# Kernel optimization log

Measured on AMD Instinct MI355X. Metric: run time of the kernel, lower is better.

The kernel has to match this reference:

```python
import jax, jax.numpy as jnp
import numpy as np
from jax import lax

N_GAUSS = 4096


def setup_inputs() -> dict:
    key = jax.random.key(0)
    k1, k2, k3, k4 = jax.random.split(key, 4)
    return {
        "_xyz": jax.random.normal(k1, (N_GAUSS, 3), dtype=jnp.float32),
        "_scaling": jax.random.normal(k2, (N_GAUSS, 3), dtype=jnp.float32),
        "_rotation": jax.random.normal(k3, (N_GAUSS, 4), dtype=jnp.float32),
        "_opacity": jax.random.normal(k4, (N_GAUSS, 1), dtype=jnp.float32),
        "resolution": 64,
        "num_blocks": 16,
    }


def _extract_fields(_xyz, _scaling, _rotation, _opacity, resolution, num_blocks):
    relax_ratio = 1.5
    block_size = 2.0 / num_blocks
    split_size = resolution // num_blocks

    # opacity activation + threshold mask (kept dense; masked gaussians get 0 weight)
    opacities = jax.nn.sigmoid(_opacity)[:, 0]  # [N]
    keep = opacities > 0.005
    opa = jnp.where(keep, opacities, 0.0)

    BIG = jnp.float32(1e10)
    mn = jnp.min(jnp.where(keep[:, None], _xyz, BIG), axis=0)
    mx = jnp.max(jnp.where(keep[:, None], _xyz, -BIG), axis=0)
    center = (mn + mx) / 2
    scale = 1.8 / jnp.max(mx - mn)
    xyzs = (_xyz - center) * scale           # [N,3] normalized positions
    stds = jnp.exp(_scaling) * scale         # [N,3] scaling activation * scale

    # covariance from scaling+rotation: L = R @ diag(s); C = L L^T
    q = _rotation / jnp.linalg.norm(_rotation, axis=1, keepdims=True)
    r, x, y, z = q[:, 0], q[:, 1], q[:, 2], q[:, 3]
    R = jnp.stack([
        jnp.stack([1 - 2 * (y * y + z * z), 2 * (x * y - r * z), 2 * (x * z + r * y)], -1),
        jnp.stack([2 * (x * y + r * z), 1 - 2 * (x * x + z * z), 2 * (y * z - r * x)], -1),
        jnp.stack([2 * (x * z - r * y), 2 * (y * z + r * x), 1 - 2 * (x * x + y * y)], -1),
    ], axis=1)                               # [N,3,3]
    L = R * stds[:, None, :]                 # R @ diag(s)
    C = jnp.einsum('nij,nkj->nik', L, L)     # [N,3,3]
    a, b, c = C[:, 0, 0], C[:, 0, 1], C[:, 0, 2]
    d, e, f = C[:, 1, 1], C[:, 1, 2], C[:, 2, 2]

    # analytic 3x3 symmetric inverse (precomputed per gaussian)
    inv_det = 1.0 / (a * d * f + 2 * e * c * b - e * e * a - c * c * d - b * b * f + 1e-24)
    inv_a = (d * f - e * e) * inv_det
    inv_b = (e * c - b * f) * inv_det
    inv_c = (e * b - c * d) * inv_det
    inv_d = (a * f - c * c) * inv_det
    inv_e = (b * c - e * a) * inv_det
    inv_f = (a * d - b * b) * inv_det

    lin = jnp.linspace(-1.0, 1.0, resolution).astype(jnp.float32)
    nb = num_blocks
    bi, bj, bk = jnp.meshgrid(jnp.arange(nb), jnp.arange(nb), jnp.arange(nb), indexing='ij')
    blocks = jnp.stack([bi.ravel(), bj.ravel(), bk.ravel()], axis=1)  # [nb^3, 3]
    off = jnp.arange(split_size)
    relax = block_size * relax_ratio

    def block_val(blk):
        xs = lin[blk[0] * split_size + off]
        ys = lin[blk[1] * split_size + off]
        zs = lin[blk[2] * split_size + off]
        xx, yy, zz = jnp.meshgrid(xs, ys, zs, indexing='ij')
        pts = jnp.stack([xx.ravel(), yy.ravel(), zz.ravel()], axis=-1)  # [S^3, 3]
        vmin = pts.min(0) - relax
        vmax = pts.max(0) + relax
        inside = jnp.all((xyzs < vmax) & (xyzs > vmin), axis=1)  # [N]
        w_opa = jnp.where(inside, opa, 0.0)                      # [N]
        dxyz = pts[:, None, :] - xyzs[None, :, :]                # [S^3, N, 3]
        px, py, pz = dxyz[..., 0], dxyz[..., 1], dxyz[..., 2]
        power = (-0.5 * (px * px * inv_a + py * py * inv_d + pz * pz * inv_f)
                 - px * py * inv_b - px * pz * inv_c - py * pz * inv_e)
        power = jnp.where(power > 0, jnp.float32(-1e10), power)
        val = jnp.sum(w_opa * jnp.exp(power), axis=1)            # [S^3]
        return val.reshape(split_size, split_size, split_size)

    vals = lax.map(block_val, blocks)  # [nb^3, S, S, S]
    occ = (vals.reshape(nb, nb, nb, split_size, split_size, split_size)
               .transpose(0, 3, 1, 4, 2, 5)
               .reshape(resolution, resolution, resolution))
    return occ


def reference(_xyz, _scaling, _rotation, _opacity, resolution, num_blocks):
    return _extract_fields(_xyz, _scaling, _rotation, _opacity, resolution, num_blocks)
```

## Files before the change

kernel.cpp:

```cpp
#include <hip/hip_runtime.h>

#define NG 4096
#define RELAX 0.1875f
#define KEEPTH -5.2933049f

__device__ __forceinline__ float linf(int i) { return -1.0f + (2.0f/63.0f)*(float)i; }
__device__ __forceinline__ int cperm(int i) { return (i & 1) ? 7 + ((i+1)>>1) : 7 - (i>>1); }

template<int T>
__device__ __forceinline__ float4 block_minmax_cs(
    const float4* __restrict__ xyz4, const float4* __restrict__ op4,
    int tid, float (*s_r)[6])
{
  float mn0=1e10f, mn1=1e10f, mn2=1e10f;
  float mx0=-1e10f, mx1=-1e10f, mx2=-1e10f;
  #pragma unroll
  for (int t = 0; t < NG/4/T; ++t) {
    const int G = t*T + tid;
    float4 v0 = xyz4[3*G+0], v1 = xyz4[3*G+1], v2 = xyz4[3*G+2];
    float4 oo = op4[G];
    if (oo.x > KEEPTH) { mn0=fminf(mn0,v0.x); mx0=fmaxf(mx0,v0.x);
                         mn1=fminf(mn1,v0.y); mx1=fmaxf(mx1,v0.y);
                         mn2=fminf(mn2,v0.z); mx2=fmaxf(mx2,v0.z); }
    if (oo.y > KEEPTH) { mn0=fminf(mn0,v0.w); mx0=fmaxf(mx0,v0.w);
                         mn1=fminf(mn1,v1.x); mx1=fmaxf(mx1,v1.x);
                         mn2=fminf(mn2,v1.y); mx2=fmaxf(mx2,v1.y); }
    if (oo.z > KEEPTH) { mn0=fminf(mn0,v1.z); mx0=fmaxf(mx0,v1.z);
                         mn1=fminf(mn1,v1.w); mx1=fmaxf(mx1,v1.w);
                         mn2=fminf(mn2,v2.x); mx2=fmaxf(mx2,v2.x); }
    if (oo.w > KEEPTH) { mn0=fminf(mn0,v2.y); mx0=fmaxf(mx0,v2.y);
                         mn1=fminf(mn1,v2.z); mx1=fmaxf(mx1,v2.z);
                         mn2=fminf(mn2,v2.w); mx2=fmaxf(mx2,v2.w); }
  }
  #pragma unroll
  for (int s = 1; s < 64; s <<= 1) {
    mn0 = fminf(mn0, __shfl_xor(mn0, s)); mx0 = fmaxf(mx0, __shfl_xor(mx0, s));
    mn1 = fminf(mn1, __shfl_xor(mn1, s)); mx1 = fmaxf(mx1, __shfl_xor(mx1, s));
    mn2 = fminf(mn2, __shfl_xor(mn2, s)); mx2 = fmaxf(mx2, __shfl_xor(mx2, s));
  }
  if ((tid & 63) == 0) {
    const int w = tid >> 6;
    s_r[w][0]=mn0; s_r[w][1]=mn1; s_r[w][2]=mn2;
    s_r[w][3]=mx0; s_r[w][4]=mx1; s_r[w][5]=mx2;
  }
  __syncthreads();
  mn0 = s_r[0][0]; mn1 = s_r[0][1]; mn2 = s_r[0][2];
  mx0 = s_r[0][3]; mx1 = s_r[0][4]; mx2 = s_r[0][5];
  #pragma unroll
  for (int w = 1; w < T/64; ++w) {
    mn0 = fminf(mn0, s_r[w][0]); mn1 = fminf(mn1, s_r[w][1]); mn2 = fminf(mn2, s_r[w][2]);
    mx0 = fmaxf(mx0, s_r[w][3]); mx1 = fmaxf(mx1, s_r[w][4]); mx2 = fmaxf(mx2, s_r[w][5]);
  }
  return make_float4((mn0+mx0)*0.5f, (mn1+mx1)*0.5f, (mn2+mx2)*0.5f,
                     1.8f/fmaxf(mx0-mn0, fmaxf(mx1-mn1, mx2-mn2)));
}

__device__ __forceinline__ void transform_one(
    const float* __restrict__ xyz, const float* __restrict__ scal,
    const float* __restrict__ rot, const float* __restrict__ opac,
    int g, float cx, float cy, float cz, float sc,
    float4* __restrict__ pos, float4* __restrict__ inv)
{
  float o = opac[g];
  float sig = 1.0f/(1.0f + __expf(-o));
  float opa = (sig > 0.005f) ? sig : 0.0f;
  float xs = (xyz[3*g+0]-cx)*sc;
  float ys = (xyz[3*g+1]-cy)*sc;
  float zs = (xyz[3*g+2]-cz)*sc;
  float sdx = __expf(scal[3*g+0])*sc;
  float sdy = __expf(scal[3*g+1])*sc;
  float sdz = __expf(scal[3*g+2])*sc;
  float qr=rot[4*g+0], qx=rot[4*g+1], qy=rot[4*g+2], qz=rot[4*g+3];
  float qn = 1.0f/sqrtf(qr*qr+qx*qx+qy*qy+qz*qz);
  qr*=qn; qx*=qn; qy*=qn; qz*=qn;
  float R00 = 1.0f-2.0f*(qy*qy+qz*qz), R01 = 2.0f*(qx*qy-qr*qz), R02 = 2.0f*(qx*qz+qr*qy);
  float R10 = 2.0f*(qx*qy+qr*qz), R11 = 1.0f-2.0f*(qx*qx+qz*qz), R12 = 2.0f*(qy*qz-qr*qx);
  float R20 = 2.0f*(qx*qz-qr*qy), R21 = 2.0f*(qy*qz+qr*qx), R22 = 1.0f-2.0f*(qx*qx+qy*qy);
  float L00=R00*sdx, L01=R01*sdy, L02=R02*sdz;
  float L10=R10*sdx, L11=R11*sdy, L12=R12*sdz;
  float L20=R20*sdx, L21=R21*sdy, L22=R22*sdz;
  float a = L00*L00+L01*L01+L02*L02;
  float bb= L00*L10+L01*L11+L02*L12;
  float cc= L00*L20+L01*L21+L02*L22;
  float d = L10*L10+L11*L11+L12*L12;
  float e = L10*L20+L11*L21+L12*L22;
  float f = L20*L20+L21*L21+L22*L22;
  float det = a*d*f + 2.0f*e*cc*bb - e*e*a - cc*cc*d - bb*bb*f + 1e-24f;
  float idt = 1.0f/det;
  float ia=(d*f-e*e)*idt, ib=(e*cc-bb*f)*idt, ic=(e*bb-cc*d)*idt;
  float id=(a*f-cc*cc)*idt, ie=(bb*cc-e*a)*idt, iff=(a*d-bb*bb)*idt;
  pos[g]     = make_float4(xs, ys, zs, opa);
  inv[2*g+0] = make_float4(-0.5f*ia, -ib, -ic, -0.5f*id);
  inv[2*g+1] = make_float4(-ie, -0.5f*iff, 0.0f, 0.0f);
}

__global__ __launch_bounds__(512) void gm_prep(
    const float* __restrict__ xyz, const float* __restrict__ scal,
    const float* __restrict__ rot, const float* __restrict__ opac,
    float4* __restrict__ pos, float4* __restrict__ inv)
{
  __shared__ float s_r[8][6];
  const int tid = threadIdx.x;
  const int b   = blockIdx.x;
  const float4* xyz4 = (const float4*)xyz;
  const float4* op4  = (const float4*)opac;
  const float4 cs = block_minmax_cs<512>(xyz4, op4, tid, s_r);
  if (tid < 16)
    transform_one(xyz, scal, rot, opac, b*16+tid, cs.x, cs.y, cs.z, cs.w, pos, inv);
}

__global__ __launch_bounds__(512) void gm_eval(
    const float4* __restrict__ pos, const float4* __restrict__ inv,
    float* __restrict__ out)
{
  __shared__ float4 s_g[8][64*3];
  __shared__ int    s_f[8][64];
  __shared__ float  s_p[8][4][64];
  const int tid  = threadIdx.x;
  const int w    = tid >> 6;
  const int lane = tid & 63;
  const int b = blockIdx.x;
  const int sx = lane >> 4, sy = (lane >> 2) & 3, sz = lane & 3;

  float vmnx[4], vmxx[4], vmny[4], vmxy[4], vmnz[4], vmxz[4];
  float ptx[4], pty[4], ptz[4];
  #pragma unroll
  for (int q = 0; q < 4; ++q) {
    const int rank = q*1024 + ((b + q*331) & 1023);
    const int bi = cperm(rank >> 8), bj = cperm((rank >> 4) & 15), bk = cperm(rank & 15);
    vmnx[q] = linf(bi*4) - RELAX; vmxx[q] = linf(bi*4+3) + RELAX;
    vmny[q] = linf(bj*4) - RELAX; vmxy[q] = linf(bj*4+3) + RELAX;
    vmnz[q] = linf(bk*4) - RELAX; vmxz[q] = linf(bk*4+3) + RELAX;
    ptx[q] = linf(bi*4+sx); pty[q] = linf(bj*4+sy); ptz[q] = linf(bk*4+sz);
  }

  float acc0 = 0.0f, acc1 = 0.0f, acc2 = 0.0f, acc3 = 0.0f;
  const int gbase = w*512 + lane;
  float4 P = pos[gbase];

  #pragma unroll
  for (int t = 0; t < 8; ++t) {
    const int g = gbase + t*64;
    float4 Pn;
    if (t < 7) Pn = pos[g + 64];
    int flags = 0;
    if (P.w > 0.0f) {
      #pragma unroll
      for (int q = 0; q < 4; ++q) {
        if (P.x > vmnx[q] && P.x < vmxx[q] &&
            P.y > vmny[q] && P.y < vmxy[q] &&
            P.z > vmnz[q] && P.z < vmxz[q]) flags |= (1 << q);
      }
    }
    const unsigned long long mask = __ballot(flags != 0);
    const int mU = __popcll(mask);
    if (mU != 0) {
      if (flags) {
        const int slot = __popcll(mask & ((1ull << lane) - 1ull));
        s_g[w][3*slot+0] = P;
        s_g[w][3*slot+1] = inv[2*g+0];
        s_g[w][3*slot+2] = inv[2*g+1];
        s_f[w][slot] = flags;
      }
      __builtin_amdgcn_wave_barrier();
      for (int s = 0; s < mU; ++s) {
        const float4 Pq = s_g[w][3*s+0];
        const float4 I0 = s_g[w][3*s+1];
        const float4 I1 = s_g[w][3*s+2];
        const int fl = s_f[w][s];
        if (fl & 1) {
          float px = ptx[0]-Pq.x, py = pty[0]-Pq.y, pz = ptz[0]-Pq.z;
          float power = px*px*I0.x + py*py*I0.w + pz*pz*I1.y
                      + px*py*I0.y + px*pz*I0.z + py*pz*I1.x;
          power = (power > 0.0f) ? -1e10f : power;
          acc0 += Pq.w * __expf(power);
        }
        if (fl & 2) {
          float px = ptx[1]-Pq.x, py = pty[1]-Pq.y, pz = ptz[1]-Pq.z;
          float power = px*px*I0.x + py*py*I0.w + pz*pz*I1.y
                      + px*py*I0.y + px*pz*I0.z + py*pz*I1.x;
          power = (power > 0.0f) ? -1e10f : power;
          acc1 += Pq.w * __expf(power);
        }
        if (fl & 4) {
          float px = ptx[2]-Pq.x, py = pty[2]-Pq.y, pz = ptz[2]-Pq.z;
          float power = px*px*I0.x + py*py*I0.w + pz*pz*I1.y
                      + px*py*I0.y + px*pz*I0.z + py*pz*I1.x;
          power = (power > 0.0f) ? -1e10f : power;
          acc2 += Pq.w * __expf(power);
        }
        if (fl & 8) {
          float px = ptx[3]-Pq.x, py = pty[3]-Pq.y, pz = ptz[3]-Pq.z;
          float power = px*px*I0.x + py*py*I0.w + pz*pz*I1.y
                      + px*py*I0.y + px*pz*I0.z + py*pz*I1.x;
          power = (power > 0.0f) ? -1e10f : power;
          acc3 += Pq.w * __expf(power);
        }
      }
      __builtin_amdgcn_wave_barrier();
    }
    P = Pn;
  }

  s_p[w][0][lane] = acc0;
  s_p[w][1][lane] = acc1;
  s_p[w][2][lane] = acc2;
  s_p[w][3][lane] = acc3;
  __syncthreads();
  if (w < 4) {
    const int rank = w*1024 + ((b + w*331) & 1023);
    const int bi = cperm(rank >> 8), bj = cperm((rank >> 4) & 15), bk = cperm(rank & 15);
    float v = 0.0f;
    #pragma unroll
    for (int u = 0; u < 8; ++u) v += s_p[u][w][lane];
    out[(bi*4+sx)*4096 + (bj*4+sy)*64 + (bk*4+sz)] = v;
  }
}

__global__ __launch_bounds__(256) void gm_fused_nows(
    const float* __restrict__ xyz, const float* __restrict__ scal,
    const float* __restrict__ rot, const float* __restrict__ opac,
    float* __restrict__ out)
{
  __shared__ float s_r[8][6];
  __shared__ float4 s_g[256*3];
  __shared__ float  s_acc[256];
  __shared__ int    s_cnt;
  const int tid = threadIdx.x;
  const float4* xyz4 = (const float4*)xyz;
  const float4* op4  = (const float4*)opac;
  if (tid == 0) s_cnt = 0;
  const float4 cs = block_minmax_cs<256>(xyz4, op4, tid, s_r);
  const float cx = cs.x, cy = cs.y, cz = cs.z, sc = cs.w;

  const int bin = blockIdx.x;
  const int bi = bin >> 8, bj = (bin >> 4) & 15, bk = bin & 15;
  const float vminx = linf(bi*4) - RELAX, vmaxx = linf(bi*4+3) + RELAX;
  const float vminy = linf(bj*4) - RELAX, vmaxy = linf(bj*4+3) + RELAX;
  const float vminz = linf(bk*4) - RELAX, vmaxz = linf(bk*4+3) + RELAX;
  const int p    = tid & 63;
  const int part = tid >> 6;
  const int sx = p >> 4, sy = (p >> 2) & 3, sz = p & 3;
  const float ptx = linf(bi*4+sx), pty = linf(bj*4+sy), ptz = linf(bk*4+sz);
  float acc = 0.0f;
  __syncthreads();

  for (int c0 = 0; c0 < NG; c0 += 256) {
    const int g = c0 + tid;
    float o = opac[g];
    bool pass = false;
    float xs=0, ys=0, zs=0, sig=0;
    if (o > KEEPTH) {
      sig = 1.0f/(1.0f + __expf(-o));
      xs = (xyz[3*g+0]-cx)*sc;
      ys = (xyz[3*g+1]-cy)*sc;
      zs = (xyz[3*g+2]-cz)*sc;
      pass = xs > vminx && xs < vmaxx &&
             ys > vminy && ys < vmaxy &&
             zs > vminz && zs < vmaxz;
    }
    if (pass) {
      float sdx = __expf(scal[3*g+0])*sc;
      float sdy = __expf(scal[3*g+1])*sc;
      float sdz = __expf(scal[3*g+2])*sc;
      float qr=rot[4*g+0], qx=rot[4*g+1], qy=rot[4*g+2], qz=rot[4*g+3];
      float qn = 1.0f/sqrtf(qr*qr+qx*qx+qy*qy+qz*qz);
      qr*=qn; qx*=qn; qy*=qn; qz*=qn;
      float R00 = 1.0f-2.0f*(qy*qy+qz*qz), R01 = 2.0f*(qx*qy-qr*qz), R02 = 2.0f*(qx*qz+qr*qy);
      float R10 = 2.0f*(qx*qy+qr*qz), R11 = 1.0f-2.0f*(qx*qx+qz*qz), R12 = 2.0f*(qy*qz-qr*qx);
      float R20 = 2.0f*(qx*qz-qr*qy), R21 = 2.0f*(qy*qz+qr*qx), R22 = 1.0f-2.0f*(qx*qx+qy*qy);
      float L00=R00*sdx, L01=R01*sdy, L02=R02*sdz;
      float L10=R10*sdx, L11=R11*sdy, L12=R12*sdz;
      float L20=R20*sdx, L21=R21*sdy, L22=R22*sdz;
      float a = L00*L00+L01*L01+L02*L02;
      float bb= L00*L10+L01*L11+L02*L12;
      float cc= L00*L20+L01*L21+L02*L22;
      float d = L10*L10+L11*L11+L12*L12;
      float e = L10*L20+L11*L21+L12*L22;
      float f = L20*L20+L21*L21+L22*L22;
      float det = a*d*f + 2.0f*e*cc*bb - e*e*a - cc*cc*d - bb*bb*f + 1e-24f;
      float idt = 1.0f/det;
      float ia=(d*f-e*e)*idt, ib=(e*cc-bb*f)*idt, ic=(e*bb-cc*d)*idt;
      float id=(a*f-cc*cc)*idt, ie=(bb*cc-e*a)*idt, iff=(a*d-bb*bb)*idt;
      int slot = atomicAdd(&s_cnt, 1);
      s_g[3*slot+0] = make_float4(xs, ys, zs, sig);
      s_g[3*slot+1] = make_float4(-0.5f*ia, -ib, -ic, -0.5f*id);
      s_g[3*slot+2] = make_float4(-ie, -0.5f*iff, 0.0f, 0.0f);
    }
    __syncthreads();
    const int nn = s_cnt;
    #pragma unroll 4
    for (int j = part; j < nn; j += 4) {
      float4 P  = s_g[3*j+0];
      float4 I0 = s_g[3*j+1];
      float4 I1 = s_g[3*j+2];
      float px = ptx - P.x, py = pty - P.y, pz = ptz - P.z;
      float power = px*px*I0.x + py*py*I0.w + pz*pz*I1.y
                  + px*py*I0.y + px*pz*I0.z + py*pz*I1.x;
      power = (power > 0.0f) ? -1e10f : power;
      acc += P.w * __expf(power);
    }
    __syncthreads();
    if (tid == 0) s_cnt = 0;
    __syncthreads();
  }
  s_acc[tid] = acc;
  __syncthreads();
  if (tid < 64) {
    float v = s_acc[tid] + s_acc[tid+64] + s_acc[tid+128] + s_acc[tid+192];
    out[(bi*4+sx)*4096 + (bj*4+sy)*64 + (bk*4+sz)] = v;
  }
}

extern "C" void kernel_launch(void* const* d_in, const int* in_sizes, int n_in,
                              void* d_out, int out_size, void* d_ws, size_t ws_size,
                              hipStream_t stream) {
  const float* xyz  = (const float*)d_in[0];
  const float* scal = (const float*)d_in[1];
  const float* rot  = (const float*)d_in[2];
  const float* opac = (const float*)d_in[3];
  float* out = (float*)d_out;
  char* ws = (char*)d_ws;
  float4* pos = (float4*)ws;
  float4* inv = (float4*)(ws + 65536);

  if (ws_size >= 196608) {
    gm_prep<<<256, 512, 0, stream>>>(xyz, scal, rot, opac, pos, inv);
    gm_eval<<<1024, 512, 0, stream>>>(pos, inv, out);
  } else {
    gm_fused_nows<<<4096, 256, 0, stream>>>(xyz, scal, rot, opac, out);
  }
}
```

Baseline: 113.5 us.

## Broadcast gaussians via readlane per block and double waves per eval block

The eval kernel stops compacting in-range gaussians into LDS. It now builds a ballot mask for each of the four voxel blocks and loops over the set bits, broadcasting each gaussian's parameters with readlane, so only gaussians that touch a given block are evaluated for it. The block size grows from 512 to 1024 threads, with each wave handling 256 gaussians instead of 512, and the final reduction sums over 16 waves. This removes LDS traffic and the per-block flag branches, but it costs many scalar readlane operations per gaussian, makes the loop scalar-serialised, and may lower occupancy with the larger blocks.

```diff
diff --git a/kernel.cpp b/kernel.cpp
--- a/kernel.cpp
+++ b/kernel.cpp
@@ -6,6 +6,8 @@
 
 __device__ __forceinline__ float linf(int i) { return -1.0f + (2.0f/63.0f)*(float)i; }
 __device__ __forceinline__ int cperm(int i) { return (i & 1) ? 7 + ((i+1)>>1) : 7 - (i>>1); }
+
+#define BCAST(x, s) __int_as_float(__builtin_amdgcn_readlane(__float_as_int(x), (s)))
 
 template<int T>
 __device__ __forceinline__ float4 block_minmax_cs(
@@ -109,13 +111,11 @@
     transform_one(xyz, scal, rot, opac, b*16+tid, cs.x, cs.y, cs.z, cs.w, pos, inv);
 }
 
-__global__ __launch_bounds__(512) void gm_eval(
+__global__ __launch_bounds__(1024) void gm_eval(
     const float4* __restrict__ pos, const float4* __restrict__ inv,
     float* __restrict__ out)
 {
-  __shared__ float4 s_g[8][64*3];
-  __shared__ int    s_f[8][64];
-  __shared__ float  s_p[8][4][64];
+  __shared__ float s_p[16][4][64];
   const int tid  = threadIdx.x;
   const int w    = tid >> 6;
   const int lane = tid & 63;
@@ -134,15 +134,15 @@
     ptx[q] = linf(bi*4+sx); pty[q] = linf(bj*4+sy); ptz[q] = linf(bk*4+sz);
   }
 
-  float acc0 = 0.0f, acc1 = 0.0f, acc2 = 0.0f, acc3 = 0.0f;
-  const int gbase = w*512 + lane;
+  float acc[4] = {0.0f, 0.0f, 0.0f, 0.0f};
+  const int gbase = w*256 + lane;
   float4 P = pos[gbase];
 
   #pragma unroll
-  for (int t = 0; t < 8; ++t) {
+  for (int t = 0; t < 4; ++t) {
     const int g = gbase + t*64;
     float4 Pn;
-    if (t < 7) Pn = pos[g + 64];
+    if (t < 3) Pn = pos[g + 64];
     int flags = 0;
     if (P.w > 0.0f) {
       #pragma unroll
@@ -152,67 +152,42 @@
             P.z > vmnz[q] && P.z < vmxz[q]) flags |= (1 << q);
       }
     }
-    const unsigned long long mask = __ballot(flags != 0);
-    const int mU = __popcll(mask);
-    if (mU != 0) {
-      if (flags) {
-        const int slot = __popcll(mask & ((1ull << lane) - 1ull));
-        s_g[w][3*slot+0] = P;
-        s_g[w][3*slot+1] = inv[2*g+0];
-        s_g[w][3*slot+2] = inv[2*g+1];
-        s_f[w][slot] = flags;
+    float4 I0 = make_float4(0,0,0,0), I1 = make_float4(0,0,0,0);
+    if (flags) { I0 = inv[2*g+0]; I1 = inv[2*g+1]; }
+    unsigned long long bm[4];
+    #pragma unroll
+    for (int q = 0; q < 4; ++q) bm[q] = __ballot((flags >> q) & 1);
+
+    #pragma unroll
+    for (int q = 0; q < 4; ++q) {
+      unsigned long long rem = bm[q];
+      while (rem) {
+        const int src = (int)__builtin_ctzll(rem);
+        rem &= rem - 1ull;
+        const float Px = BCAST(P.x, src), Py = BCAST(P.y, src);
+        const float Pz = BCAST(P.z, src), Pw = BCAST(P.w, src);
+        const float a0 = BCAST(I0.x, src), a1 = BCAST(I0.y, src);
+        const float a2 = BCAST(I0.z, src), a3 = BCAST(I0.w, src);
+        const float a4 = BCAST(I1.x, src), a5 = BCAST(I1.y, src);
+        float px = ptx[q]-Px, py = pty[q]-Py, pz = ptz[q]-Pz;
+        float power = px*px*a0 + py*py*a3 + pz*pz*a5
+                    + px*py*a1 + px*pz*a2 + py*pz*a4;
+        power = (power > 0.0f) ? -1e10f : power;
+        acc[q] += Pw * __expf(power);
       }
-      __builtin_amdgcn_wave_barrier();
-      for (int s = 0; s < mU; ++s) {
-        const float4 Pq = s_g[w][3*s+0];
-        const float4 I0 = s_g[w][3*s+1];
-        const float4 I1 = s_g[w][3*s+2];
-        const int fl = s_f[w][s];
-        if (fl & 1) {
-          float px = ptx[0]-Pq.x, py = pty[0]-Pq.y, pz = ptz[0]-Pq.z;
-          float power = px*px*I0.x + py*py*I0.w + pz*pz*I1.y
-                      + px*py*I0.y + px*pz*I0.z + py*pz*I1.x;
-          power = (power > 0.0f) ? -1e10f : power;
-          acc0 += Pq.w * __expf(power);
-        }
-        if (fl & 2) {
-          float px = ptx[1]-Pq.x, py = pty[1]-Pq.y, pz = ptz[1]-Pq.z;
-          float power = px*px*I0.x + py*py*I0.w + pz*pz*I1.y
-                      + px*py*I0.y + px*pz*I0.z + py*pz*I1.x;
-          power = (power > 0.0f) ? -1e10f : power;
-          acc1 += Pq.w * __expf(power);
-        }
-        if (fl & 4) {
-          float px = ptx[2]-Pq.x, py = pty[2]-Pq.y, pz = ptz[2]-Pq.z;
-          float power = px*px*I0.x + py*py*I0.w + pz*pz*I1.y
-                      + px*py*I0.y + px*pz*I0.z + py*pz*I1.x;
-          power = (power > 0.0f) ? -1e10f : power;
-          acc2 += Pq.w * __expf(power);
-        }
-        if (fl & 8) {
-          float px = ptx[3]-Pq.x, py = pty[3]-Pq.y, pz = ptz[3]-Pq.z;
-          float power = px*px*I0.x + py*py*I0.w + pz*pz*I1.y
-                      + px*py*I0.y + px*pz*I0.z + py*pz*I1.x;
-          power = (power > 0.0f) ? -1e10f : power;
-          acc3 += Pq.w * __expf(power);
-        }
-      }
-      __builtin_amdgcn_wave_barrier();
     }
     P = Pn;
   }
 
-  s_p[w][0][lane] = acc0;
-  s_p[w][1][lane] = acc1;
-  s_p[w][2][lane] = acc2;
-  s_p[w][3][lane] = acc3;
+  #pragma unroll
+  for (int q = 0; q < 4; ++q) s_p[w][q][lane] = acc[q];
   __syncthreads();
   if (w < 4) {
     const int rank = w*1024 + ((b + w*331) & 1023);
     const int bi = cperm(rank >> 8), bj = cperm((rank >> 4) & 15), bk = cperm(rank & 15);
     float v = 0.0f;
     #pragma unroll
-    for (int u = 0; u < 8; ++u) v += s_p[u][w][lane];
+    for (int u = 0; u < 16; ++u) v += s_p[u][w][lane];
     out[(bi*4+sx)*4096 + (bj*4+sy)*64 + (bk*4+sz)] = v;
   }
 }
@@ -326,7 +301,7 @@
 
   if (ws_size >= 196608) {
     gm_prep<<<256, 512, 0, stream>>>(xyz, scal, rot, opac, pos, inv);
-    gm_eval<<<1024, 512, 0, stream>>>(pos, inv, out);
+    gm_eval<<<1024, 1024, 0, stream>>>(pos, inv, out);
   } else {
     gm_fused_nows<<<4096, 256, 0, stream>>>(xyz, scal, rot, opac, out);
   }
```

Measured after the change: 120.0 us. 5.7% more time.
